# Performance work log

Hardware: AMD Instinct MI355X
Metric: run time of the kernel (lower is better)

## Reference

```python
import jax, jax.numpy as jnp
import numpy as np

B, T, C, H = 8, 1024, 768, 12
D = C // H  # head dim = 64

def setup_inputs() -> dict:
    key = jax.random.key(0)
    k0, k1, k2, k3, k4 = jax.random.split(key, 5)
    x = jax.random.normal(k0, (B, T, C), dtype=jnp.float32)
    # flax Dense params: kernel [in, out], bias [out]
    c_attn_kernel = jax.random.normal(k1, (C, 3 * C), dtype=jnp.float32) * (1.0 / np.sqrt(C))
    c_attn_bias = jax.random.normal(k2, (3 * C,), dtype=jnp.float32) * 0.01
    c_proj_kernel = jax.random.normal(k3, (C, C), dtype=jnp.float32) * (1.0 / np.sqrt(C))
    c_proj_bias = jax.random.normal(k4, (C,), dtype=jnp.float32) * 0.01
    return {"x": x, "c_attn_kernel": c_attn_kernel, "c_attn_bias": c_attn_bias,
            "c_proj_kernel": c_proj_kernel, "c_proj_bias": c_proj_bias}

def reference(x, c_attn_kernel, c_attn_bias, c_proj_kernel, c_proj_bias):
    Bc, Tc, Cc = x.shape
    qkv = x @ c_attn_kernel + c_attn_bias          # [B, T, 3C]
    q, k, v = jnp.split(qkv, 3, axis=-1)
    q = q.reshape(Bc, Tc, H, D).swapaxes(1, 2)     # [B, H, T, D]
    k = k.reshape(Bc, Tc, H, D).swapaxes(1, 2)
    v = v.reshape(Bc, Tc, H, D).swapaxes(1, 2)
    att = jnp.matmul(q, k.swapaxes(-2, -1)) * (1.0 / jnp.sqrt(jnp.float32(D)))  # [B, H, T, T]
    mask = jnp.tril(jnp.ones((Tc, Tc), dtype=bool)).reshape(1, 1, Tc, Tc)
    att = jnp.where(mask, att, -jnp.inf)
    att = jax.nn.softmax(att, axis=-1)
    # dropout=0.0 / train=False -> identity
    y = jnp.matmul(att, v)                          # [B, H, T, D]
    y = y.swapaxes(1, 2).reshape(Bc, Tc, Cc)        # [B, T, C]
    y = y @ c_proj_kernel + c_proj_bias
    return y
```

## Files before the change

### kernel.cpp

```cpp
#include <hip/hip_runtime.h>
#include <hip/hip_bf16.h>
#include <math.h>

#define BATCH 8
#define SEQ   1024
#define CH    768
#define NH    12
#define HD    64
#define HSZ   (BATCH * NH * SEQ * HD)

typedef __attribute__((ext_vector_type(8))) short short8;
typedef __attribute__((ext_vector_type(4))) short short4v;
typedef __attribute__((ext_vector_type(4))) float floatx4;

static __device__ inline short f2bf(float f) {
    union { float f; unsigned u; } x; x.f = f;
    unsigned r = (x.u + 0x7fffu + ((x.u >> 16) & 1u)) >> 16;
    return (short)r;
}

#define GLOAD_LDS16(g, l)                                                     \
    __builtin_amdgcn_global_load_lds(                                         \
        (const __attribute__((address_space(1))) void*)(g),                   \
        (__attribute__((address_space(3))) void*)(l), 16, 0, 0)

#define NCAST (BATCH * SEQ * CH / 1024)
#define NTA   ((3 * CH / 32) * (CH / 32))
#define NTP   ((CH / 32) * (CH / 32))

__device__ __forceinline__ void transpose_tile(
    const float* __restrict__ w, short* __restrict__ wt, int K, int N,
    int bx, int by, int tid, float (*tile)[33])
{
    const int tx = tid & 31, ty = tid >> 5;
    const int n0 = bx * 32, k0 = by * 32;
    #pragma unroll
    for (int i = 0; i < 4; i++)
        tile[ty + i * 8][tx] = w[(size_t)(k0 + ty + i * 8) * N + n0 + tx];
    __syncthreads();
    #pragma unroll
    for (int i = 0; i < 4; i++)
        wt[(size_t)(n0 + ty + i * 8) * K + k0 + tx] = f2bf(tile[tx][ty + i * 8]);
}

__global__ __launch_bounds__(256) void prep_kernel(
    const float* __restrict__ x, short* __restrict__ xb,
    const float* __restrict__ wa, short* __restrict__ wta,
    const float* __restrict__ wp, short* __restrict__ wtp)
{
    __shared__ float tile[32][33];
    const int bid = blockIdx.x, tid = threadIdx.x;
    if (bid < NCAST) {
        int i = (bid * 256 + tid) * 4;
        float4 v = *(const float4*)(x + i);
        short4v o = { f2bf(v.x), f2bf(v.y), f2bf(v.z), f2bf(v.w) };
        *(short4v*)(xb + i) = o;
    } else if (bid < NCAST + NTA) {
        int t = bid - NCAST;
        transpose_tile(wa, wta, CH, 3 * CH, t % (3 * CH / 32), t / (3 * CH / 32), tid, tile);
    } else {
        int t = bid - NCAST - NTA;
        transpose_tile(wp, wtp, CH, CH, t % (CH / 32), t / (CH / 32), tid, tile);
    }
}

template <int MODE, int BM, int BN, int NBLK, int MBX, int WPE>
__global__ __launch_bounds__(256, WPE) void gemm_bt_kernel(
    const short* __restrict__ A, const short* __restrict__ Bt,
    const float* __restrict__ bias, void* __restrict__ outv,
    int M, int N, int K)
{
    constexpr int MT  = BM / 32;
    constexpr int NT  = BN / 32;
    constexpr int ACH = BM / 64;
    constexpr int BCH = BN / 64;
    constexpr int STAGE_BYTES = (BM + BN) * 128;
    constexpr int EPI_BYTES   = (MODE == 1) ? (BN * 136 * 2) : 0;
    constexpr int LDS_BYTES   = STAGE_BYTES > EPI_BYTES ? STAGE_BYTES : EPI_BYTES;
    __shared__ __align__(16) char smem[LDS_BYTES];
    short* AsB = (short*)smem;
    short* BsB = (short*)(smem + BM * 128);

    const int tid  = threadIdx.x;
    const int lane = tid & 63;
    const int col  = lane & 15;
    const int quad = lane >> 4;
    const int wave = tid >> 6;
    const int wm = wave & 1, wn = wave >> 1;

    const int bid = blockIdx.x;
    const int j   = bid & 7;
    const int t   = bid >> 3;
    const int mb  = j * MBX + t / NBLK;
    const int nb  = t % NBLK;
    const int m0 = mb * BM, n0 = nb * BN;

    const int srow = tid >> 2;
    const int kc   = ((tid & 3) ^ (srow & 3)) * 8;
    const short* aptr[ACH];
    const short* bptr[BCH];
    #pragma unroll
    for (int c = 0; c < ACH; c++)
        aptr[c] = A + (size_t)(m0 + c * 64 + srow) * K + kc;
    #pragma unroll
    for (int c = 0; c < BCH; c++)
        bptr[c] = Bt + (size_t)(n0 + c * 64 + srow) * K + kc;

    floatx4 acc[MT][NT];
    #pragma unroll
    for (int i = 0; i < MT; i++)
        #pragma unroll
        for (int jj = 0; jj < NT; jj++)
            acc[i][jj] = (floatx4){0.f, 0.f, 0.f, 0.f};

    const int niter = K / 32;

    #pragma unroll
    for (int c = 0; c < ACH; c++) GLOAD_LDS16(aptr[c], &AsB[c * 2048 + tid * 8]);
    #pragma unroll
    for (int c = 0; c < BCH; c++) GLOAD_LDS16(bptr[c], &BsB[c * 2048 + tid * 8]);

    for (int k = 0; k < niter; k++) {
        __syncthreads();
        const int cur = k & 1, nxt = cur ^ 1;
        if (k + 1 < niter) {
            const int ko = (k + 1) * 32;
            #pragma unroll
            for (int c = 0; c < ACH; c++)
                GLOAD_LDS16(aptr[c] + ko, &AsB[nxt * BM * 32 + c * 2048 + tid * 8]);
            #pragma unroll
            for (int c = 0; c < BCH; c++)
                GLOAD_LDS16(bptr[c] + ko, &BsB[nxt * BN * 32 + c * 2048 + tid * 8]);
        }
        short8 af[MT], bf[NT];
        #pragma unroll
        for (int mt = 0; mt < MT; mt++) {
            const int row = wm * (BM / 2) + mt * 16 + col;
            af[mt] = *(const short8*)&AsB[cur * BM * 32 + row * 32 + ((quad ^ (row & 3)) << 3)];
        }
        #pragma unroll
        for (int nt = 0; nt < NT; nt++) {
            const int row = wn * (BN / 2) + nt * 16 + col;
            bf[nt] = *(const short8*)&BsB[cur * BN * 32 + row * 32 + ((quad ^ (row & 3)) << 3)];
        }
        #pragma unroll
        for (int mt = 0; mt < MT; mt++)
            #pragma unroll
            for (int nt = 0; nt < NT; nt++)
                acc[mt][nt] = __builtin_amdgcn_mfma_f32_16x16x32_bf16(
                    af[mt], bf[nt], acc[mt][nt], 0, 0, 0);
    }

    if constexpr (MODE == 0) {
        #pragma unroll
        for (int mt = 0; mt < MT; mt++) {
            #pragma unroll
            for (int r = 0; r < 4; r++) {
                const int m = m0 + wm * (BM / 2) + mt * 16 + quad * 4 + r;
                #pragma unroll
                for (int nt = 0; nt < NT; nt++) {
                    const int n = n0 + wn * (BN / 2) + nt * 16 + col;
                    ((float*)outv)[(size_t)m * N + n] = acc[mt][nt][r] + bias[n];
                }
            }
        }
    } else {
        __syncthreads();
        short* Es = (short*)smem;
        const int sel = n0 / CH;
        const int h0  = (n0 - sel * CH) >> 6;
        const int bb  = m0 >> 10;
        const int t0  = m0 & 1023;
        short* qkv = (short*)outv;

        if (sel < 2) {
            #pragma unroll
            for (int mt = 0; mt < MT; mt++)
                #pragma unroll
                for (int r = 0; r < 4; r++) {
                    const int lm = wm * (BM / 2) + mt * 16 + quad * 4 + r;
                    #pragma unroll
                    for (int nt = 0; nt < NT; nt++) {
                        const int ln = wn * (BN / 2) + nt * 16 + col;
                        Es[lm * 200 + ln] = f2bf(acc[mt][nt][r] + bias[n0 + ln]);
                    }
                }
            __syncthreads();
            #pragma unroll
            for (int it = 0; it < (BM * BN / 8) / 256; it++) {
                const int id = it * 256 + tid;
                const int hp = id >> 10, lm = (id >> 3) & 127, dc = id & 7;
                short8 v = *(const short8*)&Es[lm * 200 + hp * 64 + dc * 8];
                size_t dst = (size_t)sel * HSZ +
                    (((size_t)(bb * NH + h0 + hp)) * SEQ + t0 + lm) * HD + dc * 8;
                *(short8*)&qkv[dst] = v;
            }
        } else {
            #pragma unroll
            for (int nt = 0; nt < NT; nt++) {
                const int ln = wn * (BN / 2) + nt * 16 + col;
                const float bv = bias[n0 + ln];
                #pragma unroll
                for (int mt = 0; mt < MT; mt++) {
                    const int lm = wm * (BM / 2) + mt * 16 + quad * 4;
                    short4v pk;
                    #pragma unroll
                    for (int r = 0; r < 4; r++) pk[r] = f2bf(acc[mt][nt][r] + bv);
                    *(short4v*)&Es[ln * 136 + lm] = pk;
                }
            }
            __syncthreads();
            #pragma unroll
            for (int it = 0; it < (BM * BN / 8) / 256; it++) {
                const int id = it * 256 + tid;
                const int ln = id >> 4, tc = id & 15;
                short8 v = *(const short8*)&Es[ln * 136 + tc * 8];
                const int hp = ln >> 6, d = ln & 63;
                size_t dst = (size_t)2 * HSZ +
                    (((size_t)(bb * NH + h0 + hp)) * HD + d) * SEQ + t0 + tc * 8;
                *(short8*)&qkv[dst] = v;
            }
        }
    }
}

#define LDK 72

template <bool DIAG>
__device__ __forceinline__ void strip_step(
    const short* __restrict__ Ksh, const short* __restrict__ Vsh,
    short* __restrict__ pw, const short8* aq, floatx4* acc_o,
    floatx4& lacc, short8 bones, int col, int quad, int qrow0)
{
    floatx4 sacc[4];
    #pragma unroll
    for (int i = 0; i < 4; i++) sacc[i] = (floatx4){0.f, 0.f, 0.f, 0.f};
    #pragma unroll
    for (int s = 0; s < 2; s++)
        #pragma unroll
        for (int nt = 0; nt < 4; nt++) {
            short8 bk = *(const short8*)&Ksh[(nt * 16 + col) * LDK + s * 32 + quad * 8];
            sacc[nt] = __builtin_amdgcn_mfma_f32_16x16x32_bf16(aq[s], bk, sacc[nt], 0, 0, 0);
        }

    const float SCL = 0.18033688011112042f;
    #pragma unroll
    for (int r = 0; r < 4; r++)
        #pragma unroll
        for (int nt = 0; nt < 4; nt++) {
            float sv = sacc[nt][r] * SCL;
            if (DIAG && (nt * 16 + col) > (qrow0 + r)) sv = -INFINITY;
            float pv = __builtin_amdgcn_exp2f(sv);
            pw[(quad * 4 + r) * LDK + nt * 16 + col] =
                (short)(__builtin_bit_cast(unsigned, pv) >> 16);
        }
    __builtin_amdgcn_wave_barrier();

    short8 ap[2];
    ap[0] = *(const short8*)&pw[col * LDK + quad * 8];
    ap[1] = *(const short8*)&pw[col * LDK + 32 + quad * 8];

    #pragma unroll
    for (int s = 0; s < 2; s++) {
        #pragma unroll
        for (int nt = 0; nt < 4; nt++) {
            short8 bv = *(const short8*)&Vsh[(nt * 16 + col) * LDK + s * 32 + quad * 8];
            acc_o[nt] = __builtin_amdgcn_mfma_f32_16x16x32_bf16(ap[s], bv, acc_o[nt], 0, 0, 0);
        }
        lacc = __builtin_amdgcn_mfma_f32_16x16x32_bf16(ap[s], bones, lacc, 0, 0, 0);
    }
}

__global__ __launch_bounds__(512, 4) void attn_kernel(
    const short* __restrict__ Qg, const short* __restrict__ Kg,
    const short* __restrict__ Vg, short* __restrict__ Y)
{
    __shared__ __align__(16) short Ksh[64 * LDK];
    __shared__ __align__(16) short Vsh[64 * LDK];
    __shared__ __align__(16) short Psh[8][16 * LDK];

    const int tid  = threadIdx.x;
    const int wave = tid >> 6;
    const int lane = tid & 63;
    const int col  = lane & 15;
    const int quad = lane >> 4;
    const int bid = blockIdx.x;
    const int bh  = bid % 96;
    const int qt  = bid / 96;
    const int b = bh / NH, h = bh - b * NH;

    const size_t kqbase = (size_t)bh * SEQ * HD;
    const size_t vbase  = (size_t)bh * HD * SEQ;

    short8 aq[2];
    {
        const short* qp = Qg + kqbase +
            (size_t)(qt * 128 + wave * 16 + col) * HD + quad * 8;
        aq[0] = *(const short8*)(qp);
        aq[1] = *(const short8*)(qp + 32);
    }

    floatx4 acc_o[4];
    floatx4 lacc = (floatx4){0.f, 0.f, 0.f, 0.f};
    #pragma unroll
    for (int i = 0; i < 4; i++) acc_o[i] = (floatx4){0.f, 0.f, 0.f, 0.f};

    const short one_bf = (short)0x3F80;
    short8 bones = (col == 0)
        ? (short8){one_bf, one_bf, one_bf, one_bf, one_bf, one_bf, one_bf, one_bf}
        : (short8){0, 0, 0, 0, 0, 0, 0, 0};

    const int qrow0 = (wave & 3) * 16 + quad * 4;

    const int idx = tid * 8;
    const int row = idx >> 6, offs = idx & 63;

    short8 kreg, vreg;
    {
        const short* ksrc = Kg + kqbase;
        const short* vsrc = Vg + vbase;
        kreg = *(const short8*)&ksrc[idx];
        vreg = *(const short8*)&vsrc[(size_t)row * SEQ + offs];
    }

    const int nkt = 2 * qt + 2;
    for (int kt = 0; kt < nkt; kt++) {
        __syncthreads();
        *(short8*)&Ksh[row * LDK + offs] = kreg;
        *(short8*)&Vsh[row * LDK + offs] = vreg;
        __syncthreads();

        if (kt + 1 < nkt) {
            const short* ksrc = Kg + kqbase + (size_t)(kt + 1) * 64 * HD;
            const short* vsrc = Vg + vbase + (kt + 1) * 64;
            kreg = *(const short8*)&ksrc[idx];
            vreg = *(const short8*)&vsrc[(size_t)row * SEQ + offs];
        }

        if (kt < 2 * qt) {
            strip_step<false>(Ksh, Vsh, Psh[wave], aq, acc_o, lacc,
                              bones, col, quad, qrow0);
        } else if (kt == 2 * qt) {
            if (wave < 4)
                strip_step<true>(Ksh, Vsh, Psh[wave], aq, acc_o, lacc,
                                 bones, col, quad, qrow0);
            else
                strip_step<false>(Ksh, Vsh, Psh[wave], aq, acc_o, lacc,
                                  bones, col, quad, qrow0);
        } else {
            if (wave >= 4)
                strip_step<true>(Ksh, Vsh, Psh[wave], aq, acc_o, lacc,
                                 bones, col, quad, qrow0);
        }
    }

    #pragma unroll
    for (int r = 0; r < 4; r++) {
        float l = __shfl(lacc[r], quad * 16, 64);
        float inv = 1.f / l;
        int t = qt * 128 + wave * 16 + quad * 4 + r;
        size_t ybase = ((size_t)(b * SEQ + t)) * CH + h * HD;
        #pragma unroll
        for (int nt = 0; nt < 4; nt++)
            Y[ybase + nt * 16 + col] = f2bf(acc_o[nt][r] * inv);
    }
}

extern "C" void kernel_launch(void* const* d_in, const int* in_sizes, int n_in,
                              void* d_out, int out_size, void* d_ws, size_t ws_size,
                              hipStream_t stream)
{
    const float* x      = (const float*)d_in[0];
    const float* w_attn = (const float*)d_in[1];
    const float* b_attn = (const float*)d_in[2];
    const float* w_proj = (const float*)d_in[3];
    const float* b_proj = (const float*)d_in[4];
    float* out = (float*)d_out;

    short* qkv16 = (short*)d_ws;
    short* y16   = qkv16 + (size_t)3 * HSZ;
    short* xb    = y16   + (size_t)HSZ;
    short* wta   = xb    + (size_t)HSZ;
    short* wtp   = wta   + (size_t)3 * CH * CH;

    const int M = BATCH * SEQ;

    prep_kernel<<<NCAST + NTA + NTP, 256, 0, stream>>>(x, xb, w_attn, wta, w_proj, wtp);

    gemm_bt_kernel<1, 128, 192, 12, 8, 3><<<768, 256, 0, stream>>>(
        xb, wta, b_attn, qkv16, M, 3 * CH, CH);

    attn_kernel<<<768, 512, 0, stream>>>(qkv16, qkv16 + (size_t)HSZ,
                                         qkv16 + (size_t)2 * HSZ, y16);

    gemm_bt_kernel<0, 64, 192, 4, 16, 4><<<512, 256, 0, stream>>>(
        y16, wtp, b_proj, out, M, CH, CH);
}
```

Baseline: 171.7 us.

## Fuse fp32-to-bf16 conversion of x into QKV GEMM A-tile loads

Removes the separate x-cast pass from the prep kernel. The QKV GEMM now loads fp32 x directly through registers, converts it to bf16 and writes it to LDS, prefetching the next k-tile across the MFMA work. This avoids writing and rereading a bf16 copy of x (about 12.6MB of fp32 reads plus 6MB of writes in the prep pass). In exchange the GEMM reads twice the bytes for A, gives up the async global-to-LDS path for A, and uses more registers.

After: 173.0 us. About the same (+0.7%).

```diff
diff --git a/kernel.cpp b/kernel.cpp
--- a/kernel.cpp
+++ b/kernel.cpp
@@ -24,7 +24,6 @@
         (const __attribute__((address_space(1))) void*)(g),                   \
         (__attribute__((address_space(3))) void*)(l), 16, 0, 0)
 
-#define NCAST (BATCH * SEQ * CH / 1024)
 #define NTA   ((3 * CH / 32) * (CH / 32))
 #define NTP   ((CH / 32) * (CH / 32))
 
@@ -44,29 +43,22 @@
 }
 
 __global__ __launch_bounds__(256) void prep_kernel(
-    const float* __restrict__ x, short* __restrict__ xb,
     const float* __restrict__ wa, short* __restrict__ wta,
     const float* __restrict__ wp, short* __restrict__ wtp)
 {
     __shared__ float tile[32][33];
     const int bid = blockIdx.x, tid = threadIdx.x;
-    if (bid < NCAST) {
-        int i = (bid * 256 + tid) * 4;
-        float4 v = *(const float4*)(x + i);
-        short4v o = { f2bf(v.x), f2bf(v.y), f2bf(v.z), f2bf(v.w) };
-        *(short4v*)(xb + i) = o;
-    } else if (bid < NCAST + NTA) {
-        int t = bid - NCAST;
-        transpose_tile(wa, wta, CH, 3 * CH, t % (3 * CH / 32), t / (3 * CH / 32), tid, tile);
+    if (bid < NTA) {
+        transpose_tile(wa, wta, CH, 3 * CH, bid % (3 * CH / 32), bid / (3 * CH / 32), tid, tile);
     } else {
-        int t = bid - NCAST - NTA;
+        int t = bid - NTA;
         transpose_tile(wp, wtp, CH, CH, t % (CH / 32), t / (CH / 32), tid, tile);
     }
 }
 
 template <int MODE, int BM, int BN, int NBLK, int MBX, int WPE>
 __global__ __launch_bounds__(256, WPE) void gemm_bt_kernel(
-    const short* __restrict__ A, const short* __restrict__ Bt,
+    const void* __restrict__ Av, const short* __restrict__ Bt,
     const float* __restrict__ bias, void* __restrict__ outv,
     int M, int N, int K)
 {
@@ -97,15 +89,21 @@
 
     const int srow = tid >> 2;
     const int kc   = ((tid & 3) ^ (srow & 3)) * 8;
-    const short* aptr[ACH];
     const short* bptr[BCH];
-    #pragma unroll
-    for (int c = 0; c < ACH; c++)
-        aptr[c] = A + (size_t)(m0 + c * 64 + srow) * K + kc;
     #pragma unroll
     for (int c = 0; c < BCH; c++)
         bptr[c] = Bt + (size_t)(n0 + c * 64 + srow) * K + kc;
 
+    const float* xptr[ACH];
+    const short* aptr[ACH];
+    #pragma unroll
+    for (int c = 0; c < ACH; c++) {
+        if constexpr (MODE == 1)
+            xptr[c] = (const float*)Av + (size_t)(m0 + c * 64 + srow) * K + kc;
+        else
+            aptr[c] = (const short*)Av + (size_t)(m0 + c * 64 + srow) * K + kc;
+    }
+
     floatx4 acc[MT][NT];
     #pragma unroll
     for (int i = 0; i < MT; i++)
@@ -116,22 +114,45 @@
     const int niter = K / 32;
 
     #pragma unroll
-    for (int c = 0; c < ACH; c++) GLOAD_LDS16(aptr[c], &AsB[c * 2048 + tid * 8]);
-    #pragma unroll
     for (int c = 0; c < BCH; c++) GLOAD_LDS16(bptr[c], &BsB[c * 2048 + tid * 8]);
+    if constexpr (MODE == 1) {
+        #pragma unroll
+        for (int c = 0; c < ACH; c++) {
+            float4 f0 = *(const float4*)(xptr[c]);
+            float4 f1 = *(const float4*)(xptr[c] + 4);
+            short8 s = { f2bf(f0.x), f2bf(f0.y), f2bf(f0.z), f2bf(f0.w),
+                         f2bf(f1.x), f2bf(f1.y), f2bf(f1.z), f2bf(f1.w) };
+            *(short8*)&AsB[c * 2048 + tid * 8] = s;
+        }
+    } else {
+        #pragma unroll
+        for (int c = 0; c < ACH; c++) GLOAD_LDS16(aptr[c], &AsB[c * 2048 + tid * 8]);
+    }
 
     for (int k = 0; k < niter; k++) {
         __syncthreads();
         const int cur = k & 1, nxt = cur ^ 1;
-        if (k + 1 < niter) {
-            const int ko = (k + 1) * 32;
-            #pragma unroll
-            for (int c = 0; c < ACH; c++)
-                GLOAD_LDS16(aptr[c] + ko, &AsB[nxt * BM * 32 + c * 2048 + tid * 8]);
+        const bool pf = (k + 1 < niter);
+        const int ko = (k + 1) * 32;
+
+        float4 f0[ACH], f1[ACH];
+        if (pf) {
             #pragma unroll
             for (int c = 0; c < BCH; c++)
                 GLOAD_LDS16(bptr[c] + ko, &BsB[nxt * BN * 32 + c * 2048 + tid * 8]);
-        }
+            if constexpr (MODE == 1) {
+                #pragma unroll
+                for (int c = 0; c < ACH; c++) {
+                    f0[c] = *(const float4*)(xptr[c] + ko);
+                    f1[c] = *(const float4*)(xptr[c] + ko + 4);
+                }
+            } else {
+                #pragma unroll
+                for (int c = 0; c < ACH; c++)
+                    GLOAD_LDS16(aptr[c] + ko, &AsB[nxt * BM * 32 + c * 2048 + tid * 8]);
+            }
+        }
+
         short8 af[MT], bf[NT];
         #pragma unroll
         for (int mt = 0; mt < MT; mt++) {
@@ -149,6 +170,17 @@
             for (int nt = 0; nt < NT; nt++)
                 acc[mt][nt] = __builtin_amdgcn_mfma_f32_16x16x32_bf16(
                     af[mt], bf[nt], acc[mt][nt], 0, 0, 0);
+
+        if constexpr (MODE == 1) {
+            if (pf) {
+                #pragma unroll
+                for (int c = 0; c < ACH; c++) {
+                    short8 s = { f2bf(f0[c].x), f2bf(f0[c].y), f2bf(f0[c].z), f2bf(f0[c].w),
+                                 f2bf(f1[c].x), f2bf(f1[c].y), f2bf(f1[c].z), f2bf(f1[c].w) };
+                    *(short8*)&AsB[nxt * BM * 32 + c * 2048 + tid * 8] = s;
+                }
+            }
+        }
     }
 
     if constexpr (MODE == 0) {
@@ -379,16 +411,15 @@
 
     short* qkv16 = (short*)d_ws;
     short* y16   = qkv16 + (size_t)3 * HSZ;
-    short* xb    = y16   + (size_t)HSZ;
-    short* wta   = xb    + (size_t)HSZ;
+    short* wta   = y16   + (size_t)HSZ;
     short* wtp   = wta   + (size_t)3 * CH * CH;
 
     const int M = BATCH * SEQ;
 
-    prep_kernel<<<NCAST + NTA + NTP, 256, 0, stream>>>(x, xb, w_attn, wta, w_proj, wtp);
+    prep_kernel<<<NTA + NTP, 256, 0, stream>>>(w_attn, wta, w_proj, wtp);
 
     gemm_bt_kernel<1, 128, 192, 12, 8, 3><<<768, 256, 0, stream>>>(
-        xb, wta, b_attn, qkv16, M, 3 * CH, CH);
+        x, wta, b_attn, qkv16, M, 3 * CH, CH);
 
     attn_kernel<<<768, 512, 0, stream>>>(qkv16, qkv16 + (size_t)HSZ,
                                          qkv16 + (size_t)2 * HSZ, y16);
```
